# Kernel optimization log

Measured on AMD Instinct MI355X. Metric: run time of the kernel, lower is better.

The kernel has to match this reference:

```python
import jax, jax.numpy as jnp
import numpy as np

EMBED_DIM = 128
NUM_HEADS = 16
D_K = EMBED_DIM // NUM_HEADS  # 8 qubits per head
DEPTH = 2

# Sign matrix for PauliZ expectations: wire w corresponds to bit (D_K-1-w) of the
# flattened state index (wire 0 = most significant axis, torchquantum convention).
_idx = np.arange(2 ** D_K)
_SIGNS = np.stack([1.0 - 2.0 * ((_idx >> (D_K - 1 - w)) & 1) for w in range(D_K)], axis=1).astype(np.float32)  # [2^d_k, d_k]


def quantum_layer(tokens, qparams):
    """Simulate the variational circuit for a batch of tokens.
    tokens: [N, d_k] real angles; qparams: [depth, d_k] trainable RX angles.
    RX(a)RX(b)=RX(a+b) on the same wire, so encoder + all depth RX layers
    compose into a single RX per wire. Then `depth` CNOT ladders, then <Z_w>.
    """
    theta = tokens + jnp.sum(qparams, axis=0)  # [N, d_k]
    half = 0.5 * theta
    # single-qubit amplitudes after RX(theta)|0>: [cos(t/2), -i sin(t/2)]
    amp = jnp.stack([jnp.cos(half).astype(jnp.complex64),
                     (-1j) * jnp.sin(half).astype(jnp.complex64)], axis=-1)  # [N, d_k, 2]
    # build product state [N, 2, 2, ..., 2]
    state = amp[:, 0, :]
    for i in range(1, D_K):
        state = jnp.einsum('n...,nq->n...q', state, amp[:, i, :])
    # depth x CNOT ladder: CNOT(i, i+1) for i in 0..d_k-2
    for _ in range(DEPTH):
        for i in range(D_K - 1):
            c_ax = 1 + i
            c0 = jnp.take(state, 0, axis=c_ax)
            c1 = jnp.take(state, 1, axis=c_ax)
            c1 = jnp.flip(c1, axis=c_ax)  # target axis = c_ax+1, shifted by -1 after take
            state = jnp.stack([c0, c1], axis=c_ax)
    probs = (state.real ** 2 + state.imag ** 2).reshape(state.shape[0], -1)  # [N, 2^d_k]
    return probs @ jnp.asarray(_SIGNS)  # [N, d_k]


def setup_inputs() -> dict:
    key = jax.random.key(0)
    ks = jax.random.split(key, 6)
    B, S, E = 4, 512, EMBED_DIM
    scale = 1.0 / np.sqrt(E)
    return {
        'x': jax.random.normal(ks[0], (B, S, E), dtype=jnp.float32),
        'Wq': jax.random.normal(ks[1], (E, E), dtype=jnp.float32) * scale,
        'Wk': jax.random.normal(ks[2], (E, E), dtype=jnp.float32) * scale,
        'Wv': jax.random.normal(ks[3], (E, E), dtype=jnp.float32) * scale,
        'Wo': jax.random.normal(ks[4], (E, E), dtype=jnp.float32) * scale,
        'qparams': jax.random.normal(ks[5], (DEPTH, D_K), dtype=jnp.float32),
    }


def reference(x, Wq, Wk, Wv, Wo, qparams):
    B, S, E = x.shape
    H, dk = NUM_HEADS, D_K
    # linear projections (torch Linear, no bias): y = x @ W.T
    q = (x @ Wq.T).reshape(B, S, H, dk).transpose(0, 2, 1, 3)  # [B,H,S,dk]
    k = (x @ Wk.T).reshape(B, S, H, dk).transpose(0, 2, 1, 3)
    v = (x @ Wv.T).reshape(B, S, H, dk).transpose(0, 2, 1, 3)
    # batched quantum circuit over all (batch, head, seq) tokens; shared weights
    qq = quantum_layer(q.reshape(-1, dk), qparams).reshape(B, H, S, dk)
    kq = quantum_layer(k.reshape(-1, dk), qparams).reshape(B, H, S, dk)
    vq = quantum_layer(v.reshape(-1, dk), qparams).reshape(B, H, S, dk)
    scores = jnp.einsum('bhqd,bhkd->bhqk', qq, kq) / jnp.sqrt(jnp.float32(dk))
    attn = jax.nn.softmax(scores, axis=-1)  # dropout in eval mode: identity
    out = jnp.einsum('bhqk,bhkd->bhqd', attn, vq)
    out = out.transpose(0, 2, 1, 3).reshape(B, S, E)
    return out @ Wo.T
```

## Files before the change

### kernel.cpp

```cpp
#include <hip/hip_runtime.h>
#include <cmath>

#define MATSZ 262144
#define WT_OFF 0
#define QKV_OFF 65536
#define AOUT_OFF (65536 + 3 * MATSZ)

__global__ __launch_bounds__(256) void k_prep(
    const float* __restrict__ Wq, const float* __restrict__ Wk,
    const float* __restrict__ Wv, const float* __restrict__ Wo,
    float* __restrict__ ws) {
  __shared__ float s[32][33];
  const int m = blockIdx.y;
  const int tr = blockIdx.x >> 2;
  const int tc = blockIdx.x & 3;
  const float* W = (m == 0) ? Wq : (m == 1) ? Wk : (m == 2) ? Wv : Wo;
  const int lk = threadIdx.x & 31;
  const int l0 = threadIdx.x >> 5;
#pragma unroll
  for (int i = 0; i < 4; ++i) {
    int lc = l0 + i * 8;
    s[lc][lk] = W[(size_t)(tr * 32 + lc) * 128 + tc * 32 + lk];
  }
  __syncthreads();
  float* wt = ws + WT_OFF + m * 16384;
#pragma unroll
  for (int i = 0; i < 4; ++i) {
    int lkk = l0 + i * 8;
    wt[(size_t)(tc * 32 + lkk) * 128 + tr * 32 + lk] = s[lk][lkk];
  }
}

__global__ __launch_bounds__(256, 4) void k_qkvq(
    const float* __restrict__ x, const float* __restrict__ qp,
    float* __restrict__ ws) {
  __shared__ float xs[16][128];
  const int t = threadIdx.x;
  const int tile = blockIdx.x;
  const int m = blockIdx.y;
  {
    const float4* xg = (const float4*)(x + (size_t)tile * 2048);
    float4* xv = (float4*)&xs[0][0];
    xv[t] = xg[t];
    xv[t + 256] = xg[t + 256];
  }
  __syncthreads();
  const int cg = t & 31, rg = t >> 5;
  const float4* wt4 = (const float4*)(ws + WT_OFF + m * 16384);
  const float4* xs4 = (const float4*)&xs[0][0];
  float4 acc0 = make_float4(0.f, 0.f, 0.f, 0.f);
  float4 acc1 = make_float4(0.f, 0.f, 0.f, 0.f);
#pragma unroll 4
  for (int kc = 0; kc < 32; ++kc) {
    float4 w0 = wt4[(kc * 4 + 0) * 32 + cg];
    float4 w1 = wt4[(kc * 4 + 1) * 32 + cg];
    float4 w2 = wt4[(kc * 4 + 2) * 32 + cg];
    float4 w3 = wt4[(kc * 4 + 3) * 32 + cg];
    float4 xa = xs4[(rg * 2 + 0) * 32 + kc];
    float4 xb = xs4[(rg * 2 + 1) * 32 + kc];
    acc0.x = fmaf(xa.x, w0.x, acc0.x); acc0.y = fmaf(xa.x, w0.y, acc0.y);
    acc0.z = fmaf(xa.x, w0.z, acc0.z); acc0.w = fmaf(xa.x, w0.w, acc0.w);
    acc0.x = fmaf(xa.y, w1.x, acc0.x); acc0.y = fmaf(xa.y, w1.y, acc0.y);
    acc0.z = fmaf(xa.y, w1.z, acc0.z); acc0.w = fmaf(xa.y, w1.w, acc0.w);
    acc0.x = fmaf(xa.z, w2.x, acc0.x); acc0.y = fmaf(xa.z, w2.y, acc0.y);
    acc0.z = fmaf(xa.z, w2.z, acc0.z); acc0.w = fmaf(xa.z, w2.w, acc0.w);
    acc0.x = fmaf(xa.w, w3.x, acc0.x); acc0.y = fmaf(xa.w, w3.y, acc0.y);
    acc0.z = fmaf(xa.w, w3.z, acc0.z); acc0.w = fmaf(xa.w, w3.w, acc0.w);
    acc1.x = fmaf(xb.x, w0.x, acc1.x); acc1.y = fmaf(xb.x, w0.y, acc1.y);
    acc1.z = fmaf(xb.x, w0.z, acc1.z); acc1.w = fmaf(xb.x, w0.w, acc1.w);
    acc1.x = fmaf(xb.y, w1.x, acc1.x); acc1.y = fmaf(xb.y, w1.y, acc1.y);
    acc1.z = fmaf(xb.y, w1.z, acc1.z); acc1.w = fmaf(xb.y, w1.w, acc1.w);
    acc1.x = fmaf(xb.z, w2.x, acc1.x); acc1.y = fmaf(xb.z, w2.y, acc1.y);
    acc1.z = fmaf(xb.z, w2.z, acc1.z); acc1.w = fmaf(xb.z, w2.w, acc1.w);
    acc1.x = fmaf(xb.w, w3.x, acc1.x); acc1.y = fmaf(xb.w, w3.y, acc1.y);
    acc1.z = fmaf(xb.w, w3.z, acc1.z); acc1.w = fmaf(xb.w, w3.w, acc1.w);
  }
  const int j0 = (cg & 1) * 4;
  float4 qs;
  qs.x = qp[j0 + 0] + qp[8 + j0 + 0];
  qs.y = qp[j0 + 1] + qp[8 + j0 + 1];
  qs.z = qp[j0 + 2] + qp[8 + j0 + 2];
  qs.w = qp[j0 + 3] + qp[8 + j0 + 3];
  const int h = cg >> 1;
  const bool hi = (cg & 1) != 0;
#pragma unroll
  for (int r = 0; r < 2; ++r) {
    float4 a = (r == 0) ? acc0 : acc1;
    float4 c;
    c.x = __cosf(a.x + qs.x);
    c.y = __cosf(a.y + qs.y);
    c.z = __cosf(a.z + qs.z);
    c.w = __cosf(a.w + qs.w);
    float4 u;
    u.x = c.x; u.y = c.y; u.z = c.x * c.z; u.w = c.y * c.w;
    float gz = __shfl_xor(u.z, 1);
    float gw = __shfl_xor(u.w, 1);
    float mz = hi ? gz : 1.f, mw = hi ? gw : 1.f;
    float4 o;
    o.x = u.x * mz; o.y = u.y * mw; o.z = u.z * mz; o.w = u.w * mw;
    int row = tile * 16 + rg * 2 + r;
    int b = row >> 9, s = row & 511;
    float* dst = ws + QKV_OFF + (size_t)m * MATSZ +
                 ((size_t)((b << 4) + h) * 512 + s) * 8 + (hi ? 4 : 0);
    *(float4*)dst = o;
  }
}

__global__ __launch_bounds__(256, 4) void k_attn(
    float* __restrict__ ws) {
  __shared__ float4 kslo[512], kshi[512], vslo[512], vshi[512];
  const int qt = blockIdx.x;
  const int bh = blockIdx.y;
  const float* qkv = ws + QKV_OFF;
  const float* Qg = qkv + (size_t)bh * 4096;
  const float4* Kg = (const float4*)(qkv + MATSZ + (size_t)bh * 4096);
  const float4* Vg = (const float4*)(qkv + 2 * (size_t)MATSZ + (size_t)bh * 4096);
  const int t = threadIdx.x;
  for (int k = t; k < 512; k += 256) {
    kslo[k] = Kg[2 * k]; kshi[k] = Kg[2 * k + 1];
    vslo[k] = Vg[2 * k]; vshi[k] = Vg[2 * k + 1];
  }
  __syncthreads();
  const int qslot = t >> 4, ko = t & 15;
  const int row0 = qt * 64 + qslot * 4;
  const float scale = 0.35355339059327373f;
  float4 qa[4], qb[4];
#pragma unroll
  for (int r = 0; r < 4; ++r) {
    qa[r] = ((const float4*)(Qg + (size_t)(row0 + r) * 8))[0];
    qb[r] = ((const float4*)(Qg + (size_t)(row0 + r) * 8))[1];
    qa[r].x *= scale; qa[r].y *= scale; qa[r].z *= scale; qa[r].w *= scale;
    qb[r].x *= scale; qb[r].y *= scale; qb[r].z *= scale; qb[r].w *= scale;
  }
  float l[4] = {0.f, 0.f, 0.f, 0.f};
  float a[4][8];
#pragma unroll
  for (int r = 0; r < 4; ++r)
#pragma unroll
    for (int j = 0; j < 8; ++j) a[r][j] = 0.f;
#pragma unroll 2
  for (int i = 0; i < 32; ++i) {
    int k = i * 16 + ko;
    float4 kx = kslo[k], ky = kshi[k];
    float4 vx = vslo[k], vy = vshi[k];
#pragma unroll
    for (int r = 0; r < 4; ++r) {
      float s = qa[r].x * kx.x + qa[r].y * kx.y + qa[r].z * kx.z + qa[r].w * kx.w +
                qb[r].x * ky.x + qb[r].y * ky.y + qb[r].z * ky.z + qb[r].w * ky.w;
      float p = __expf(s);
      l[r] += p;
      a[r][0] = fmaf(p, vx.x, a[r][0]);
      a[r][1] = fmaf(p, vx.y, a[r][1]);
      a[r][2] = fmaf(p, vx.z, a[r][2]);
      a[r][3] = fmaf(p, vx.w, a[r][3]);
      a[r][4] = fmaf(p, vy.x, a[r][4]);
      a[r][5] = fmaf(p, vy.y, a[r][5]);
      a[r][6] = fmaf(p, vy.z, a[r][6]);
      a[r][7] = fmaf(p, vy.w, a[r][7]);
    }
  }
#pragma unroll
  for (int mm = 1; mm <= 8; mm <<= 1) {
#pragma unroll
    for (int r = 0; r < 4; ++r) {
      l[r] += __shfl_xor(l[r], mm);
#pragma unroll
      for (int j = 0; j < 8; ++j) a[r][j] += __shfl_xor(a[r][j], mm);
    }
  }
  if (ko == 0) {
    int b = bh >> 4, h = bh & 15;
    float* aout = ws + AOUT_OFF;
#pragma unroll
    for (int r = 0; r < 4; ++r) {
      float inv = 1.f / l[r];
      float* d = aout + ((size_t)(b * 512 + row0 + r)) * 128 + h * 8;
      ((float4*)d)[0] = make_float4(a[r][0] * inv, a[r][1] * inv,
                                    a[r][2] * inv, a[r][3] * inv);
      ((float4*)d)[1] = make_float4(a[r][4] * inv, a[r][5] * inv,
                                    a[r][6] * inv, a[r][7] * inv);
    }
  }
}

__global__ __launch_bounds__(256, 4) void k_out(
    const float* __restrict__ ws, float* __restrict__ out) {
  __shared__ float as_[16][128];
  const int t = threadIdx.x;
  const int tile = blockIdx.x;
  const float* aout = ws + AOUT_OFF;
  {
    const float4* ag = (const float4*)(aout + (size_t)tile * 2048);
    float4* av = (float4*)&as_[0][0];
    av[t] = ag[t];
    av[t + 256] = ag[t + 256];
  }
  __syncthreads();
  const int cg = t & 31, rg = t >> 5;
  const float4* wt4 = (const float4*)(ws + WT_OFF + 3 * 16384);
  const float4* as4 = (const float4*)&as_[0][0];
  float4 acc0 = make_float4(0.f, 0.f, 0.f, 0.f);
  float4 acc1 = make_float4(0.f, 0.f, 0.f, 0.f);
#pragma unroll 4
  for (int kc = 0; kc < 32; ++kc) {
    float4 w0 = wt4[(kc * 4 + 0) * 32 + cg];
    float4 w1 = wt4[(kc * 4 + 1) * 32 + cg];
    float4 w2 = wt4[(kc * 4 + 2) * 32 + cg];
    float4 w3 = wt4[(kc * 4 + 3) * 32 + cg];
    float4 xa = as4[(rg * 2 + 0) * 32 + kc];
    float4 xb = as4[(rg * 2 + 1) * 32 + kc];
    acc0.x = fmaf(xa.x, w0.x, acc0.x); acc0.y = fmaf(xa.x, w0.y, acc0.y);
    acc0.z = fmaf(xa.x, w0.z, acc0.z); acc0.w = fmaf(xa.x, w0.w, acc0.w);
    acc0.x = fmaf(xa.y, w1.x, acc0.x); acc0.y = fmaf(xa.y, w1.y, acc0.y);
    acc0.z = fmaf(xa.y, w1.z, acc0.z); acc0.w = fmaf(xa.y, w1.w, acc0.w);
    acc0.x = fmaf(xa.z, w2.x, acc0.x); acc0.y = fmaf(xa.z, w2.y, acc0.y);
    acc0.z = fmaf(xa.z, w2.z, acc0.z); acc0.w = fmaf(xa.z, w2.w, acc0.w);
    acc0.x = fmaf(xa.w, w3.x, acc0.x); acc0.y = fmaf(xa.w, w3.y, acc0.y);
    acc0.z = fmaf(xa.w, w3.z, acc0.z); acc0.w = fmaf(xa.w, w3.w, acc0.w);
    acc1.x = fmaf(xb.x, w0.x, acc1.x); acc1.y = fmaf(xb.x, w0.y, acc1.y);
    acc1.z = fmaf(xb.x, w0.z, acc1.z); acc1.w = fmaf(xb.x, w0.w, acc1.w);
    acc1.x = fmaf(xb.y, w1.x, acc1.x); acc1.y = fmaf(xb.y, w1.y, acc1.y);
    acc1.z = fmaf(xb.y, w1.z, acc1.z); acc1.w = fmaf(xb.y, w1.w, acc1.w);
    acc1.x = fmaf(xb.z, w2.x, acc1.x); acc1.y = fmaf(xb.z, w2.y, acc1.y);
    acc1.z = fmaf(xb.z, w2.z, acc1.z); acc1.w = fmaf(xb.z, w2.w, acc1.w);
    acc1.x = fmaf(xb.w, w3.x, acc1.x); acc1.y = fmaf(xb.w, w3.y, acc1.y);
    acc1.z = fmaf(xb.w, w3.z, acc1.z); acc1.w = fmaf(xb.w, w3.w, acc1.w);
  }
  const int row = tile * 16 + rg * 2;
  ((float4*)(out + (size_t)row * 128))[cg] = acc0;
  ((float4*)(out + (size_t)(row + 1) * 128))[cg] = acc1;
}

extern "C" void kernel_launch(void* const* d_in, const int* in_sizes, int n_in,
                              void* d_out, int out_size, void* d_ws, size_t ws_size,
                              hipStream_t stream) {
  const float* x  = (const float*)d_in[0];
  const float* Wq = (const float*)d_in[1];
  const float* Wk = (const float*)d_in[2];
  const float* Wv = (const float*)d_in[3];
  const float* Wo = (const float*)d_in[4];
  const float* qp = (const float*)d_in[5];
  float* out = (float*)d_out;
  float* ws = (float*)d_ws;

  hipLaunchKernelGGL(k_prep, dim3(16, 4), dim3(256), 0, stream,
                     Wq, Wk, Wv, Wo, ws);
  hipLaunchKernelGGL(k_qkvq, dim3(128, 3), dim3(256), 0, stream, x, qp, ws);
  hipLaunchKernelGGL(k_attn, dim3(8, 64), dim3(256), 0, stream, ws);
  hipLaunchKernelGGL(k_out, dim3(128), dim3(256), 0, stream, ws, out);
}
```

Before: 45.96 us.

## Drop weight-transpose prep kernel; read untransposed weights into registers with split-K

Removes the k_prep launch that transposed the weight matrices into the workspace. The projection kernels now hold one weight row per thread (half of K) in 16 float4 registers and compute dot products against 8 shared-memory token rows. Two half-K partial sums are reduced through shared memory. This saves a kernel launch and a global round trip, and doubles the grid size. In exchange it uses more registers per thread (launch bounds lowered to 3) and reloads each weight row in every block.

```diff
diff --git a/kernel.cpp b/kernel.cpp
--- a/kernel.cpp
+++ b/kernel.cpp
@@ -2,108 +2,76 @@
 #include <cmath>
 
 #define MATSZ 262144
-#define WT_OFF 0
 #define QKV_OFF 65536
 #define AOUT_OFF (65536 + 3 * MATSZ)
 
-__global__ __launch_bounds__(256) void k_prep(
-    const float* __restrict__ Wq, const float* __restrict__ Wk,
-    const float* __restrict__ Wv, const float* __restrict__ Wo,
-    float* __restrict__ ws) {
-  __shared__ float s[32][33];
-  const int m = blockIdx.y;
-  const int tr = blockIdx.x >> 2;
-  const int tc = blockIdx.x & 3;
-  const float* W = (m == 0) ? Wq : (m == 1) ? Wk : (m == 2) ? Wv : Wo;
-  const int lk = threadIdx.x & 31;
-  const int l0 = threadIdx.x >> 5;
-#pragma unroll
-  for (int i = 0; i < 4; ++i) {
-    int lc = l0 + i * 8;
-    s[lc][lk] = W[(size_t)(tr * 32 + lc) * 128 + tc * 32 + lk];
-  }
-  __syncthreads();
-  float* wt = ws + WT_OFF + m * 16384;
-#pragma unroll
-  for (int i = 0; i < 4; ++i) {
-    int lkk = l0 + i * 8;
-    wt[(size_t)(tc * 32 + lkk) * 128 + tr * 32 + lk] = s[lk][lkk];
-  }
-}
-
-__global__ __launch_bounds__(256, 4) void k_qkvq(
-    const float* __restrict__ x, const float* __restrict__ qp,
-    float* __restrict__ ws) {
-  __shared__ float xs[16][128];
+__global__ __launch_bounds__(256, 3) void k_qkvq(
+    const float* __restrict__ x, const float* __restrict__ Wq,
+    const float* __restrict__ Wk, const float* __restrict__ Wv,
+    const float* __restrict__ qp, float* __restrict__ ws) {
+  __shared__ float xs[8][128];
+  __shared__ float th[2][8][128];
   const int t = threadIdx.x;
   const int tile = blockIdx.x;
   const int m = blockIdx.y;
-  {
-    const float4* xg = (const float4*)(x + (size_t)tile * 2048);
-    float4* xv = (float4*)&xs[0][0];
-    xv[t] = xg[t];
-    xv[t + 256] = xg[t + 256];
+  const float* W = (m == 0) ? Wq : (m == 1) ? Wk : Wv;
+  {
+    ((float4*)&xs[0][0])[t] = ((const float4*)(x + (size_t)tile * 1024))[t];
+  }
+  const int e = t & 127, half = t >> 7;
+  float4 w[16];
+  {
+    const float4* wr = (const float4*)W + (size_t)e * 32 + half * 16;
+#pragma unroll
+    for (int i = 0; i < 16; ++i) w[i] = wr[i];
+  }
+  __syncthreads();
+  const float4* xs4 = (const float4*)&xs[0][0];
+#pragma unroll
+  for (int r = 0; r < 8; ++r) {
+    float a = 0.f;
+    const float4* xr = xs4 + r * 32 + half * 16;
+#pragma unroll
+    for (int i = 0; i < 16; ++i) {
+      float4 xv = xr[i];
+      a = fmaf(xv.x, w[i].x, a);
+      a = fmaf(xv.y, w[i].y, a);
+      a = fmaf(xv.z, w[i].z, a);
+      a = fmaf(xv.w, w[i].w, a);
+    }
+    th[half][r][e] = a;
   }
   __syncthreads();
   const int cg = t & 31, rg = t >> 5;
-  const float4* wt4 = (const float4*)(ws + WT_OFF + m * 16384);
-  const float4* xs4 = (const float4*)&xs[0][0];
-  float4 acc0 = make_float4(0.f, 0.f, 0.f, 0.f);
-  float4 acc1 = make_float4(0.f, 0.f, 0.f, 0.f);
-#pragma unroll 4
-  for (int kc = 0; kc < 32; ++kc) {
-    float4 w0 = wt4[(kc * 4 + 0) * 32 + cg];
-    float4 w1 = wt4[(kc * 4 + 1) * 32 + cg];
-    float4 w2 = wt4[(kc * 4 + 2) * 32 + cg];
-    float4 w3 = wt4[(kc * 4 + 3) * 32 + cg];
-    float4 xa = xs4[(rg * 2 + 0) * 32 + kc];
-    float4 xb = xs4[(rg * 2 + 1) * 32 + kc];
-    acc0.x = fmaf(xa.x, w0.x, acc0.x); acc0.y = fmaf(xa.x, w0.y, acc0.y);
-    acc0.z = fmaf(xa.x, w0.z, acc0.z); acc0.w = fmaf(xa.x, w0.w, acc0.w);
-    acc0.x = fmaf(xa.y, w1.x, acc0.x); acc0.y = fmaf(xa.y, w1.y, acc0.y);
-    acc0.z = fmaf(xa.y, w1.z, acc0.z); acc0.w = fmaf(xa.y, w1.w, acc0.w);
-    acc0.x = fmaf(xa.z, w2.x, acc0.x); acc0.y = fmaf(xa.z, w2.y, acc0.y);
-    acc0.z = fmaf(xa.z, w2.z, acc0.z); acc0.w = fmaf(xa.z, w2.w, acc0.w);
-    acc0.x = fmaf(xa.w, w3.x, acc0.x); acc0.y = fmaf(xa.w, w3.y, acc0.y);
-    acc0.z = fmaf(xa.w, w3.z, acc0.z); acc0.w = fmaf(xa.w, w3.w, acc0.w);
-    acc1.x = fmaf(xb.x, w0.x, acc1.x); acc1.y = fmaf(xb.x, w0.y, acc1.y);
-    acc1.z = fmaf(xb.x, w0.z, acc1.z); acc1.w = fmaf(xb.x, w0.w, acc1.w);
-    acc1.x = fmaf(xb.y, w1.x, acc1.x); acc1.y = fmaf(xb.y, w1.y, acc1.y);
-    acc1.z = fmaf(xb.y, w1.z, acc1.z); acc1.w = fmaf(xb.y, w1.w, acc1.w);
-    acc1.x = fmaf(xb.z, w2.x, acc1.x); acc1.y = fmaf(xb.z, w2.y, acc1.y);
-    acc1.z = fmaf(xb.z, w2.z, acc1.z); acc1.w = fmaf(xb.z, w2.w, acc1.w);
-    acc1.x = fmaf(xb.w, w3.x, acc1.x); acc1.y = fmaf(xb.w, w3.y, acc1.y);
-    acc1.z = fmaf(xb.w, w3.z, acc1.z); acc1.w = fmaf(xb.w, w3.w, acc1.w);
-  }
+  const float4* th4 = (const float4*)&th[0][0][0];
+  float4 s0 = th4[rg * 32 + cg];
+  float4 s1 = th4[256 + rg * 32 + cg];
+  float4 a4 = make_float4(s0.x + s1.x, s0.y + s1.y, s0.z + s1.z, s0.w + s1.w);
   const int j0 = (cg & 1) * 4;
   float4 qs;
   qs.x = qp[j0 + 0] + qp[8 + j0 + 0];
   qs.y = qp[j0 + 1] + qp[8 + j0 + 1];
   qs.z = qp[j0 + 2] + qp[8 + j0 + 2];
   qs.w = qp[j0 + 3] + qp[8 + j0 + 3];
+  float4 c;
+  c.x = __cosf(a4.x + qs.x);
+  c.y = __cosf(a4.y + qs.y);
+  c.z = __cosf(a4.z + qs.z);
+  c.w = __cosf(a4.w + qs.w);
+  float4 u;
+  u.x = c.x; u.y = c.y; u.z = c.x * c.z; u.w = c.y * c.w;
+  float gz = __shfl_xor(u.z, 1);
+  float gw = __shfl_xor(u.w, 1);
+  const bool hi = (cg & 1) != 0;
+  float mz = hi ? gz : 1.f, mw = hi ? gw : 1.f;
+  float4 o;
+  o.x = u.x * mz; o.y = u.y * mw; o.z = u.z * mz; o.w = u.w * mw;
   const int h = cg >> 1;
-  const bool hi = (cg & 1) != 0;
-#pragma unroll
-  for (int r = 0; r < 2; ++r) {
-    float4 a = (r == 0) ? acc0 : acc1;
-    float4 c;
-    c.x = __cosf(a.x + qs.x);
-    c.y = __cosf(a.y + qs.y);
-    c.z = __cosf(a.z + qs.z);
-    c.w = __cosf(a.w + qs.w);
-    float4 u;
-    u.x = c.x; u.y = c.y; u.z = c.x * c.z; u.w = c.y * c.w;
-    float gz = __shfl_xor(u.z, 1);
-    float gw = __shfl_xor(u.w, 1);
-    float mz = hi ? gz : 1.f, mw = hi ? gw : 1.f;
-    float4 o;
-    o.x = u.x * mz; o.y = u.y * mw; o.z = u.z * mz; o.w = u.w * mw;
-    int row = tile * 16 + rg * 2 + r;
-    int b = row >> 9, s = row & 511;
-    float* dst = ws + QKV_OFF + (size_t)m * MATSZ +
-                 ((size_t)((b << 4) + h) * 512 + s) * 8 + (hi ? 4 : 0);
-    *(float4*)dst = o;
-  }
+  int row = tile * 8 + rg;
+  int b = row >> 9, s = row & 511;
+  float* dst = ws + QKV_OFF + (size_t)m * MATSZ +
+               ((size_t)((b << 4) + h) * 512 + s) * 8 + (hi ? 4 : 0);
+  *(float4*)dst = o;
 }
 
 __global__ __launch_bounds__(256, 4) void k_attn(
@@ -183,52 +151,47 @@
   }
 }
 
-__global__ __launch_bounds__(256, 4) void k_out(
-    const float* __restrict__ ws, float* __restrict__ out) {
-  __shared__ float as_[16][128];
+__global__ __launch_bounds__(256, 3) void k_out(
+    const float* __restrict__ ws, const float* __restrict__ Wo,
+    float* __restrict__ out) {
+  __shared__ float as_[8][128];
+  __shared__ float th[2][8][128];
   const int t = threadIdx.x;
   const int tile = blockIdx.x;
   const float* aout = ws + AOUT_OFF;
   {
-    const float4* ag = (const float4*)(aout + (size_t)tile * 2048);
-    float4* av = (float4*)&as_[0][0];
-    av[t] = ag[t];
-    av[t + 256] = ag[t + 256];
+    ((float4*)&as_[0][0])[t] = ((const float4*)(aout + (size_t)tile * 1024))[t];
+  }
+  const int e = t & 127, half = t >> 7;
+  float4 w[16];
+  {
+    const float4* wr = (const float4*)Wo + (size_t)e * 32 + half * 16;
+#pragma unroll
+    for (int i = 0; i < 16; ++i) w[i] = wr[i];
+  }
+  __syncthreads();
+  const float4* as4 = (const float4*)&as_[0][0];
+#pragma unroll
+  for (int r = 0; r < 8; ++r) {
+    float a = 0.f;
+    const float4* ar = as4 + r * 32 + half * 16;
+#pragma unroll
+    for (int i = 0; i < 16; ++i) {
+      float4 av = ar[i];
+      a = fmaf(av.x, w[i].x, a);
+      a = fmaf(av.y, w[i].y, a);
+      a = fmaf(av.z, w[i].z, a);
+      a = fmaf(av.w, w[i].w, a);
+    }
+    th[half][r][e] = a;
   }
   __syncthreads();
   const int cg = t & 31, rg = t >> 5;
-  const float4* wt4 = (const float4*)(ws + WT_OFF + 3 * 16384);
-  const float4* as4 = (const float4*)&as_[0][0];
-  float4 acc0 = make_float4(0.f, 0.f, 0.f, 0.f);
-  float4 acc1 = make_float4(0.f, 0.f, 0.f, 0.f);
-#pragma unroll 4
-  for (int kc = 0; kc < 32; ++kc) {
-    float4 w0 = wt4[(kc * 4 + 0) * 32 + cg];
-    float4 w1 = wt4[(kc * 4 + 1) * 32 + cg];
-    float4 w2 = wt4[(kc * 4 + 2) * 32 + cg];
-    float4 w3 = wt4[(kc * 4 + 3) * 32 + cg];
-    float4 xa = as4[(rg * 2 + 0) * 32 + kc];
-    float4 xb = as4[(rg * 2 + 1) * 32 + kc];
-    acc0.x = fmaf(xa.x, w0.x, acc0.x); acc0.y = fmaf(xa.x, w0.y, acc0.y);
-    acc0.z = fmaf(xa.x, w0.z, acc0.z); acc0.w = fmaf(xa.x, w0.w, acc0.w);
-    acc0.x = fmaf(xa.y, w1.x, acc0.x); acc0.y = fmaf(xa.y, w1.y, acc0.y);
-    acc0.z = fmaf(xa.y, w1.z, acc0.z); acc0.w = fmaf(xa.y, w1.w, acc0.w);
-    acc0.x = fmaf(xa.z, w2.x, acc0.x); acc0.y = fmaf(xa.z, w2.y, acc0.y);
-    acc0.z = fmaf(xa.z, w2.z, acc0.z); acc0.w = fmaf(xa.z, w2.w, acc0.w);
-    acc0.x = fmaf(xa.w, w3.x, acc0.x); acc0.y = fmaf(xa.w, w3.y, acc0.y);
-    acc0.z = fmaf(xa.w, w3.z, acc0.z); acc0.w = fmaf(xa.w, w3.w, acc0.w);
-    acc1.x = fmaf(xb.x, w0.x, acc1.x); acc1.y = fmaf(xb.x, w0.y, acc1.y);
-    acc1.z = fmaf(xb.x, w0.z, acc1.z); acc1.w = fmaf(xb.x, w0.w, acc1.w);
-    acc1.x = fmaf(xb.y, w1.x, acc1.x); acc1.y = fmaf(xb.y, w1.y, acc1.y);
-    acc1.z = fmaf(xb.y, w1.z, acc1.z); acc1.w = fmaf(xb.y, w1.w, acc1.w);
-    acc1.x = fmaf(xb.z, w2.x, acc1.x); acc1.y = fmaf(xb.z, w2.y, acc1.y);
-    acc1.z = fmaf(xb.z, w2.z, acc1.z); acc1.w = fmaf(xb.z, w2.w, acc1.w);
-    acc1.x = fmaf(xb.w, w3.x, acc1.x); acc1.y = fmaf(xb.w, w3.y, acc1.y);
-    acc1.z = fmaf(xb.w, w3.z, acc1.z); acc1.w = fmaf(xb.w, w3.w, acc1.w);
-  }
-  const int row = tile * 16 + rg * 2;
-  ((float4*)(out + (size_t)row * 128))[cg] = acc0;
-  ((float4*)(out + (size_t)(row + 1) * 128))[cg] = acc1;
+  const float4* th4 = (const float4*)&th[0][0][0];
+  float4 s0 = th4[rg * 32 + cg];
+  float4 s1 = th4[256 + rg * 32 + cg];
+  float4 o = make_float4(s0.x + s1.x, s0.y + s1.y, s0.z + s1.z, s0.w + s1.w);
+  ((float4*)(out + (size_t)(tile * 8 + rg) * 128))[cg] = o;
 }
 
 extern "C" void kernel_launch(void* const* d_in, const int* in_sizes, int n_in,
@@ -243,9 +206,8 @@
   float* out = (float*)d_out;
   float* ws = (float*)d_ws;
 
-  hipLaunchKernelGGL(k_prep, dim3(16, 4), dim3(256), 0, stream,
-                     Wq, Wk, Wv, Wo, ws);
-  hipLaunchKernelGGL(k_qkvq, dim3(128, 3), dim3(256), 0, stream, x, qp, ws);
+  hipLaunchKernelGGL(k_qkvq, dim3(256, 3), dim3(256), 0, stream,
+                     x, Wq, Wk, Wv, qp, ws);
   hipLaunchKernelGGL(k_attn, dim3(8, 64), dim3(256), 0, stream, ws);
-  hipLaunchKernelGGL(k_out, dim3(128), dim3(256), 0, stream, ws, out);
-}
+  hipLaunchKernelGGL(k_out, dim3(256), dim3(256), 0, stream, ws, Wo, out);
+}
```

New measurement: 41.61 us. 9.5% less time.
